# Kernel optimization log

Hardware: AMD Instinct MI355X
Metric: run time of the kernel (lower is better)

Reference implementation:

```python
import jax, jax.numpy as jnp
import numpy as np

B, P, H, D = 32, 384, 384, 512
DA, DC, DH, NUM_LABELS = 512, 512, 512, 3


def setup_inputs() -> dict:
    key = jax.random.key(0)
    ks = jax.random.split(key, 12)
    s = lambda d: 1.0 / np.sqrt(d)
    return {
        "embedded_premise": jax.random.normal(ks[0], (B, P, D), jnp.float32),
        "embedded_hypothesis": jax.random.normal(ks[1], (B, H, D), jnp.float32),
        "premise_mask": jax.random.randint(ks[2], (B, P), 0, 2, jnp.int32),
        "hypothesis_mask": jax.random.randint(ks[3], (B, H), 0, 2, jnp.int32),
        "W_attend": jax.random.normal(ks[4], (D, DA), jnp.float32) * s(D),
        "b_attend": jnp.zeros((DA,), jnp.float32),
        "W_compare": jax.random.normal(ks[5], (2 * D, DC), jnp.float32) * s(2 * D),
        "b_compare": jnp.zeros((DC,), jnp.float32),
        "W_agg1": jax.random.normal(ks[6], (2 * DC, DH), jnp.float32) * s(2 * DC),
        "b_agg1": jnp.zeros((DH,), jnp.float32),
        "W_agg2": jax.random.normal(ks[7], (DH, NUM_LABELS), jnp.float32) * s(DH),
        "b_agg2": jnp.zeros((NUM_LABELS,), jnp.float32),
    }


def masked_softmax(scores, mask):
    # AllenNLP (legacy, non-memory-efficient) masked_softmax:
    # softmax(scores * mask), re-mask, renormalize with epsilon.
    result = jax.nn.softmax(scores * mask, axis=-1)
    result = result * mask
    return result / (jnp.sum(result, axis=-1, keepdims=True) + 1e-13)


def reference(embedded_premise, embedded_hypothesis, premise_mask, hypothesis_mask,
              W_attend, b_attend, W_compare, b_compare,
              W_agg1, b_agg1, W_agg2, b_agg2):
    pm = premise_mask.astype(jnp.float32)      # [B, P]
    hm = hypothesis_mask.astype(jnp.float32)   # [B, H]

    # TimeDistributed attend feedforward (shared weights)
    proj_p = jax.nn.relu(embedded_premise @ W_attend + b_attend)      # [B, P, DA]
    proj_h = jax.nn.relu(embedded_hypothesis @ W_attend + b_attend)   # [B, H, DA]

    # Dot-product similarity matrix [B, P, H]
    sim = jnp.einsum('bpd,bhd->bph', proj_p, proj_h)

    # Cross attention with masked softmax
    p2h = masked_softmax(sim, hm[:, None, :])                          # [B, P, H]
    attended_hypothesis = jnp.einsum('bph,bhd->bpd', p2h, embedded_hypothesis)
    h2p = masked_softmax(jnp.swapaxes(sim, 1, 2), pm[:, None, :])      # [B, H, P]
    attended_premise = jnp.einsum('bhp,bpd->bhd', h2p, embedded_premise)

    # Compare feedforward on concatenated inputs, then masked sum over time
    cmp_p = jax.nn.relu(
        jnp.concatenate([embedded_premise, attended_hypothesis], axis=-1) @ W_compare + b_compare)
    compared_premise = jnp.sum(cmp_p * pm[:, :, None], axis=1)         # [B, DC]
    cmp_h = jax.nn.relu(
        jnp.concatenate([embedded_hypothesis, attended_premise], axis=-1) @ W_compare + b_compare)
    compared_hypothesis = jnp.sum(cmp_h * hm[:, :, None], axis=1)      # [B, DC]

    # Aggregate feedforward
    agg = jnp.concatenate([compared_premise, compared_hypothesis], axis=-1)
    hidden = jax.nn.relu(agg @ W_agg1 + b_agg1)
    label_logits = hidden @ W_agg2 + b_agg2                            # [B, NUM_LABELS]
    label_probs = jax.nn.softmax(label_logits, axis=-1)
    return label_logits, label_probs, h2p, p2h
```

## Files before the change

kernel.cpp:

```cpp
#include <hip/hip_runtime.h>
#include <hip/hip_bf16.h>
#include <math.h>

typedef __bf16 bf16_t;
typedef __bf16 bf16x8 __attribute__((ext_vector_type(8)));
typedef float f32x4 __attribute__((ext_vector_type(4)));

#define NPH 12288
#define SIM_B (384*384)
#define EMB_B (384*512)

#define OUT_LOGITS 0
#define OUT_PROBS 96
#define OUT_H2P 192
#define OUT_P2H (192 + 32*384*384)

#define OFF_WATH 0L
#define OFF_WATL 524288L
#define OFF_WCT  1048576L
#define OFF_A    2097152L
#define OFF_SIM  52428800L
#define OFF_CM   71303168L
#define OFF_CS   (OFF_CM + 49152L)
#define OFF_GP   (OFF_CS + 49152L)
#define OFF_H    (OFF_GP + 524288L)

#define PROJ_LO   6291456L
#define PROJ_Z    12582912L
#define ATT_ALL_E 12582912L
#define CMP_Z     6291456L

#define BM 128
#define BN 128
#define BKK 32

#define M_PROJ   0
#define M_SPLITB 1
#define M_PLAIN  2
#define M_CONCAT 3
#define O_F32   0
#define O_BF16  1
#define O_SPLIT 2
#define O_GSUM  3

__device__ inline void gload16(const void* g, void* l) {
    __builtin_amdgcn_global_load_lds(
        (const __attribute__((address_space(1))) void*)g,
        (__attribute__((address_space(3))) void*)l, 16, 0, 0);
}

template<bool SPLIT>
__device__ inline void stage_sw(const float* __restrict__ s,
                                bf16_t* hi, bf16_t* lo, int row, int c0)
{
    float xs[16];
    *(float4*)&xs[0]  = *(const float4*)(s);
    *(float4*)&xs[4]  = *(const float4*)(s + 4);
    *(float4*)&xs[8]  = *(const float4*)(s + 8);
    *(float4*)&xs[12] = *(const float4*)(s + 12);
    bf16x8 h0, h1, l0, l1;
    #pragma unroll
    for (int i = 0; i < 8; i++) {
        float x = xs[i];     bf16_t hh = (bf16_t)x; h0[i] = hh;
        float y = xs[i + 8]; bf16_t hy = (bf16_t)y; h1[i] = hy;
        if (SPLIT) { l0[i] = (bf16_t)(x - (float)hh); l1[i] = (bf16_t)(y - (float)hy); }
    }
    const int key = (row >> 1) & 3;
    const int cc0 = c0 ^ key, cc1 = cc0 ^ 1;
    *(bf16x8*)&hi[row * 32 + cc0 * 8] = h0;
    *(bf16x8*)&hi[row * 32 + cc1 * 8] = h1;
    if (SPLIT) {
        *(bf16x8*)&lo[row * 32 + cc0 * 8] = l0;
        *(bf16x8*)&lo[row * 32 + cc1 * 8] = l1;
    }
}

template<int MODE, int OUTK, bool BIAS, bool RELU>
__global__ __launch_bounds__(256) void mgemm(
    const float* __restrict__ Af, const float* __restrict__ Af2, int zalt,
    const bf16_t* __restrict__ Abh, long loA,
    const bf16_t* __restrict__ A2b, long a2B,
    const bf16_t* __restrict__ Bbh, long loB,
    const float* __restrict__ bias,
    const int* __restrict__ pmask, const int* __restrict__ hmask,
    float* __restrict__ Cf, bf16_t* __restrict__ Cb, long loC,
    int K, int K1,
    long aB, long bB, long cB,
    int lda, int lda2, int ldb, int ldc)
{
    constexpr int NS = (MODE == M_PROJ || MODE == M_SPLITB) ? 2 : 1;
    __shared__ bf16_t As[NS][BM * BKK];
    __shared__ bf16_t Bs[NS][BM * BKK];

    const int tid = threadIdx.x;

    const int gx = gridDim.x, gy = gridDim.y;
    const int nwg = gx * gy * gridDim.z;
    int flat = blockIdx.x + gx * (blockIdx.y + gy * blockIdx.z);
    flat = (flat & 7) * (nwg >> 3) + (flat >> 3);
    const int bz_ = flat / (gx * gy);
    const int rem_ = flat - bz_ * (gx * gy);
    const int by_ = rem_ / gx, bx_ = rem_ - by_ * gx;

    const long z = bz_;
    const int m0 = by_ * BM, n0 = bx_ * BN;

    const float* Afs = (MODE == M_PROJ || MODE == M_PLAIN || MODE == M_CONCAT)
                       ? ((z >= zalt) ? Af2 : Af) : nullptr;

    const int sr = tid >> 1, sc = (tid & 1) * 16, c0 = (tid & 1) * 2;
    const int gr = tid >> 2;
    const int gco = ((tid & 3) ^ ((gr >> 1) & 3)) * 8;
    const int wlds = (tid >> 6) * 512;

    const int l = tid & 63;
    const int wv = tid >> 6;
    const int wr = (wv >> 1) * 64, wc = (wv & 1) * 64;
    const int fr = l & 15, fq = l >> 4;

    f32x4 acc[4][4] = {};

    for (int k0 = 0; k0 < K; k0 += BKK) {
        if (MODE == M_PROJ || MODE == M_PLAIN) {
            const float* s = Afs + z * aB + (long)(m0 + sr) * lda + k0 + sc;
            stage_sw<MODE == M_PROJ>(s, As[0], As[NS - 1], sr, c0);
        } else if (MODE == M_CONCAT) {
            if (k0 < K1) {
                const float* s = Afs + z * aB + (long)(m0 + sr) * lda + k0 + sc;
                stage_sw<false>(s, As[0], nullptr, sr, c0);
            } else {
                const bf16_t* s = A2b + z * a2B + (long)(m0 + gr) * lda2 + (k0 - K1) + gco;
                gload16(s, &As[0][wlds]);
                gload16(s + (long)64 * lda2, &As[0][2048 + wlds]);
            }
        } else {
            const bf16_t* s = Abh + z * aB + (long)(m0 + gr) * lda + k0 + gco;
            gload16(s, &As[0][wlds]);
            gload16(s + (long)64 * lda, &As[0][2048 + wlds]);
            gload16(s + loA, &As[NS - 1][wlds]);
            gload16(s + loA + (long)64 * lda, &As[NS - 1][2048 + wlds]);
        }
        {
            const bf16_t* s = Bbh + z * bB + (long)(n0 + gr) * ldb + k0 + gco;
            gload16(s, &Bs[0][wlds]);
            gload16(s + (long)64 * ldb, &Bs[0][2048 + wlds]);
            if (NS == 2) {
                gload16(s + loB, &Bs[NS - 1][wlds]);
                gload16(s + loB + (long)64 * ldb, &Bs[NS - 1][2048 + wlds]);
            }
        }
        __syncthreads();

        bf16x8 a_h[4], b_h[4], a_l[4], b_l[4];
        #pragma unroll
        for (int i = 0; i < 4; i++) {
            const int ra = wr + i * 16 + fr;
            const int rb = wc + i * 16 + fr;
            const int ka = (fq ^ ((ra >> 1) & 3)) * 8;
            const int kb = (fq ^ ((rb >> 1) & 3)) * 8;
            a_h[i] = *(const bf16x8*)&As[0][ra * 32 + ka];
            b_h[i] = *(const bf16x8*)&Bs[0][rb * 32 + kb];
            if (NS == 2) {
                a_l[i] = *(const bf16x8*)&As[NS - 1][ra * 32 + ka];
                b_l[i] = *(const bf16x8*)&Bs[NS - 1][rb * 32 + kb];
            }
        }
        #pragma unroll
        for (int mi = 0; mi < 4; mi++)
            #pragma unroll
            for (int ni = 0; ni < 4; ni++) {
                acc[mi][ni] = __builtin_amdgcn_mfma_f32_16x16x32_bf16(a_h[mi], b_h[ni], acc[mi][ni], 0, 0, 0);
                if (NS == 2) {
                    acc[mi][ni] = __builtin_amdgcn_mfma_f32_16x16x32_bf16(a_h[mi], b_l[ni], acc[mi][ni], 0, 0, 0);
                    acc[mi][ni] = __builtin_amdgcn_mfma_f32_16x16x32_bf16(a_l[mi], b_h[ni], acc[mi][ni], 0, 0, 0);
                }
            }
        __syncthreads();
    }

    if constexpr (OUTK == O_GSUM) {
        __shared__ float red[8][128];
        __shared__ int smask[128];
        const int* mrow = (z >= zalt) ? hmask : pmask;
        const int bb = m0 / 384;
        const int brow0 = m0 - bb * 384;
        if (tid < 128) smask[tid] = mrow[bb * 384 + brow0 + tid];
        __syncthreads();
        const int rid = (wv >> 1) * 4 + fq;
        #pragma unroll
        for (int ni = 0; ni < 4; ni++) {
            const int c = wc + ni * 16 + fr;
            const float bv = bias[n0 + c];
            float local = 0.f;
            #pragma unroll
            for (int mi = 0; mi < 4; mi++)
                #pragma unroll
                for (int j = 0; j < 4; j++) {
                    const int rloc = wr + mi * 16 + fq * 4 + j;
                    float v = fmaxf(acc[mi][ni][j] + bv, 0.f);
                    local += v * (float)smask[rloc];
                }
            red[rid][c] = local;
        }
        __syncthreads();
        if (tid < 128) {
            float s = 0.f;
            #pragma unroll
            for (int r = 0; r < 8; r++) s += red[r][tid];
            const int pc = (m0 >> 7) % 3;
            Cf[((long)pc * 32 + bb) * 1024 + z * 512 + n0 + tid] = s;
        }
    } else {
        #pragma unroll
        for (int ni = 0; ni < 4; ni++) {
            const int col = n0 + wc + ni * 16 + fr;
            const float bv = BIAS ? bias[col] : 0.f;
            #pragma unroll
            for (int mi = 0; mi < 4; mi++) {
                #pragma unroll
                for (int j = 0; j < 4; j++) {
                    const int row = m0 + wr + mi * 16 + fq * 4 + j;
                    float v = acc[mi][ni][j] + bv;
                    if (RELU) v = fmaxf(v, 0.f);
                    const long idx = z * cB + (long)row * ldc + col;
                    if (OUTK == O_F32) Cf[idx] = v;
                    else if (OUTK == O_BF16) Cb[idx] = (bf16_t)v;
                    else {
                        bf16_t h = (bf16_t)v;
                        Cb[idx] = h;
                        Cb[idx + loC] = (bf16_t)(v - (float)h);
                    }
                }
            }
        }
    }
}

template<bool SPLIT>
__global__ __launch_bounds__(256) void transpose_kernel(
    const float* __restrict__ in, const float* __restrict__ in2, int zsplit,
    bf16_t* __restrict__ out, bf16_t* __restrict__ outLo,
    int R, int C, long inB, long outB)
{
    __shared__ float tile[32][33];
    const int z = blockIdx.z;
    const float* src = (z >= zsplit) ? (in2 + (long)(z - zsplit) * inB)
                                     : (in + (long)z * inB);
    const int x0 = blockIdx.x * 32, y0 = blockIdx.y * 32;
    const int tx = threadIdx.x & 31, ty = threadIdx.x >> 5;
    #pragma unroll
    for (int i = 0; i < 32; i += 8)
        tile[ty + i][tx] = src[(long)(y0 + ty + i) * C + x0 + tx];
    __syncthreads();
    bf16_t* dst = out + (long)z * outB;
    bf16_t* dstL = SPLIT ? (outLo + (long)z * outB) : nullptr;
    #pragma unroll
    for (int i = 0; i < 32; i += 8) {
        float v = tile[tx][ty + i];
        bf16_t h = (bf16_t)v;
        dst[(long)(x0 + ty + i) * R + y0 + tx] = h;
        if (SPLIT) dstL[(long)(x0 + ty + i) * R + y0 + tx] = (bf16_t)(v - (float)h);
    }
}

__global__ __launch_bounds__(384) void masked_softmax_row(
    const float* __restrict__ S, const int* __restrict__ mask,
    float* __restrict__ out)
{
    const int row = blockIdx.x;
    const int b = row / 384;
    const int t = threadIdx.x;
    __shared__ float redmax[6], redsum[6];

    float v = S[(long)row * 384 + t];
    int mm = mask[b * 384 + t];

    float x = mm ? v : -3.4e38f;
    #pragma unroll
    for (int o = 32; o > 0; o >>= 1) x = fmaxf(x, __shfl_xor(x, o, 64));
    int wid = t >> 6, lane = t & 63;
    if (lane == 0) redmax[wid] = x;
    __syncthreads();
    float mx = redmax[0];
    #pragma unroll
    for (int w = 1; w < 6; w++) mx = fmaxf(mx, redmax[w]);

    float e = mm ? expf(v - mx) : 0.f;
    float s = e;
    #pragma unroll
    for (int o = 32; o > 0; o >>= 1) s += __shfl_xor(s, o, 64);
    if (lane == 0) redsum[wid] = s;
    __syncthreads();
    float tot = 0.f;
    #pragma unroll
    for (int w = 0; w < 6; w++) tot += redsum[w];

    out[(long)row * 384 + t] = (tot > 0.f) ? e / tot : 0.f;
}

__global__ __launch_bounds__(256) void col_stats(
    const float* __restrict__ S, const int* __restrict__ mask,
    float* __restrict__ cmax, float* __restrict__ csum)
{
    __shared__ int pml[384];
    __shared__ float mred[4][64], sred[4][64];
    const int b = blockIdx.y;
    const int h0 = blockIdx.x * 64;
    const int t = threadIdx.x;
    const int tk = t >> 6, hh = t & 63;

    for (int i = t; i < 384; i += 256) pml[i] = mask[b * 384 + i];
    __syncthreads();

    const float* Sb = S + (long)b * SIM_B + h0 + hh;
    float m = -3.4e38f;
    for (int p = tk; p < 384; p += 4)
        if (pml[p]) m = fmaxf(m, Sb[(long)p * 384]);
    mred[tk][hh] = m;
    __syncthreads();
    const float M = fmaxf(fmaxf(mred[0][hh], mred[1][hh]),
                          fmaxf(mred[2][hh], mred[3][hh]));
    float s = 0.f;
    for (int p = tk; p < 384; p += 4)
        if (pml[p]) s += expf(Sb[(long)p * 384] - M);
    sred[tk][hh] = s;
    __syncthreads();
    if (t < 64) {
        const float Mf = fmaxf(fmaxf(mred[0][t], mred[1][t]),
                               fmaxf(mred[2][t], mred[3][t]));
        cmax[b * 384 + h0 + t] = Mf;
        csum[b * 384 + h0 + t] = sred[0][t] + sred[1][t] + sred[2][t] + sred[3][t];
    }
}

__global__ __launch_bounds__(256) void col_write(
    const float* __restrict__ S, const int* __restrict__ mask,
    const float* __restrict__ cmax, const float* __restrict__ csum,
    float* __restrict__ out)
{
    __shared__ float tile[32][33];
    const int b = blockIdx.z;
    const int h0 = blockIdx.x * 32, p0 = blockIdx.y * 32;
    const int tx = threadIdx.x & 31, ty = threadIdx.x >> 5;
    const float* src = S + (long)b * SIM_B;
    #pragma unroll
    for (int i = 0; i < 32; i += 8)
        tile[ty + i][tx] = src[(long)(p0 + ty + i) * 384 + h0 + tx];
    __syncthreads();
    const int pm_v = mask[b * 384 + p0 + tx];
    float* dst = out + (long)b * SIM_B;
    #pragma unroll
    for (int i = 0; i < 32; i += 8) {
        const int h = h0 + ty + i;
        const float mx = cmax[b * 384 + h];
        const float tot = csum[b * 384 + h];
        float v = tile[tx][ty + i];
        float r = (pm_v && tot > 0.f) ? expf(v - mx) / tot : 0.f;
        dst[(long)h * 384 + p0 + tx] = r;
    }
}

__global__ __launch_bounds__(256) void hidden_kernel(
    const float* __restrict__ Gp, const float* __restrict__ W1,
    const float* __restrict__ b1, float* __restrict__ Hbuf)
{
    __shared__ float g[1024];
    __shared__ float part[4][64];
    const int b = blockIdx.y, j0 = blockIdx.x * 64;
    const int t = threadIdx.x;
    for (int i = t; i < 1024; i += 256)
        g[i] = Gp[((long)0 * 32 + b) * 1024 + i] + Gp[((long)1 * 32 + b) * 1024 + i]
             + Gp[((long)2 * 32 + b) * 1024 + i];
    __syncthreads();
    const int tj = t & 63, tk = t >> 6;
    const float* w = W1 + (long)(tk * 256) * 512 + j0 + tj;
    const float* gk = g + tk * 256;
    float acc = 0.f;
    #pragma unroll 8
    for (int k = 0; k < 256; k++)
        acc = fmaf(gk[k], w[(long)k * 512], acc);
    part[tk][tj] = acc;
    __syncthreads();
    if (t < 64) {
        float v = part[0][t] + part[1][t] + part[2][t] + part[3][t] + b1[j0 + t];
        Hbuf[(long)b * 512 + j0 + t] = fmaxf(v, 0.f);
    }
}

__global__ __launch_bounds__(64) void logits_kernel(
    const float* __restrict__ Hbuf, const float* __restrict__ W2,
    const float* __restrict__ b2, float* __restrict__ out)
{
    const int b = blockIdx.x, l = threadIdx.x;
    const float* h = Hbuf + (long)b * 512;
    float a0 = 0.f, a1 = 0.f, a2 = 0.f;
    #pragma unroll
    for (int k = l; k < 512; k += 64) {
        float hv = h[k];
        a0 = fmaf(hv, W2[k * 3 + 0], a0);
        a1 = fmaf(hv, W2[k * 3 + 1], a1);
        a2 = fmaf(hv, W2[k * 3 + 2], a2);
    }
    #pragma unroll
    for (int o = 32; o > 0; o >>= 1) {
        a0 += __shfl_xor(a0, o, 64);
        a1 += __shfl_xor(a1, o, 64);
        a2 += __shfl_xor(a2, o, 64);
    }
    if (l == 0) {
        float l0 = a0 + b2[0], l1 = a1 + b2[1], l2 = a2 + b2[2];
        float mx = fmaxf(l0, fmaxf(l1, l2));
        float e0 = expf(l0 - mx), e1 = expf(l1 - mx), e2 = expf(l2 - mx);
        float s = e0 + e1 + e2;
        out[OUT_LOGITS + b * 3 + 0] = l0;
        out[OUT_LOGITS + b * 3 + 1] = l1;
        out[OUT_LOGITS + b * 3 + 2] = l2;
        out[OUT_PROBS + b * 3 + 0] = e0 / s;
        out[OUT_PROBS + b * 3 + 1] = e1 / s;
        out[OUT_PROBS + b * 3 + 2] = e2 / s;
    }
}

extern "C" void kernel_launch(void* const* d_in, const int* in_sizes, int n_in,
                              void* d_out, int out_size, void* d_ws, size_t ws_size,
                              hipStream_t stream) {
    const float* emb_p = (const float*)d_in[0];
    const float* emb_h = (const float*)d_in[1];
    const int* pm = (const int*)d_in[2];
    const int* hm = (const int*)d_in[3];
    const float* Wa = (const float*)d_in[4];
    const float* ba = (const float*)d_in[5];
    const float* Wc = (const float*)d_in[6];
    const float* bc = (const float*)d_in[7];
    const float* W1 = (const float*)d_in[8];
    const float* b1 = (const float*)d_in[9];
    const float* W2 = (const float*)d_in[10];
    const float* b2 = (const float*)d_in[11];
    float* out = (float*)d_out;
    char* W = (char*)d_ws;

    bf16_t* WaTh  = (bf16_t*)(W + OFF_WATH);
    bf16_t* WaTl  = (bf16_t*)(W + OFF_WATL);
    bf16_t* WcT   = (bf16_t*)(W + OFF_WCT);
    bf16_t* A     = (bf16_t*)(W + OFF_A);
    float*  sim   = (float*)(W + OFF_SIM);
    float*  cmaxb = (float*)(W + OFF_CM);
    float*  csumb = (float*)(W + OFF_CS);
    float*  Gp    = (float*)(W + OFF_GP);
    float*  Hbuf  = (float*)(W + OFF_H);
    bf16_t* projs  = A;
    bf16_t* embT   = A;
    bf16_t* attAll = A + ATT_ALL_E;

    transpose_kernel<true><<<dim3(16, 16, 1), 256, 0, stream>>>(
        Wa, nullptr, 999, WaTh, WaTl, 512, 512, 0, 0);
    transpose_kernel<false><<<dim3(16, 32, 1), 256, 0, stream>>>(
        Wc, nullptr, 999, WcT, nullptr, 1024, 512, 0, 0);

    mgemm<M_PROJ, O_SPLIT, true, true><<<dim3(4, 96, 2), 256, 0, stream>>>(
        emb_p, emb_h, 1, nullptr, 0, nullptr, 0, WaTh, 262144L, ba,
        nullptr, nullptr,
        nullptr, projs, PROJ_LO,
        512, 0, 0L, 0L, PROJ_Z, 512, 0, 512, 512);

    mgemm<M_SPLITB, O_F32, false, false><<<dim3(3, 3, 32), 256, 0, stream>>>(
        nullptr, nullptr, 999, projs, PROJ_LO, nullptr, 0,
        projs + PROJ_Z, PROJ_LO, nullptr,
        nullptr, nullptr,
        sim, nullptr, 0,
        512, 0, (long)EMB_B, (long)EMB_B, (long)SIM_B, 512, 0, 512, 384);

    masked_softmax_row<<<NPH, 384, 0, stream>>>(sim, hm, out + OUT_P2H);
    col_stats<<<dim3(6, 32), 256, 0, stream>>>(sim, pm, cmaxb, csumb);
    col_write<<<dim3(12, 12, 32), 256, 0, stream>>>(sim, pm, cmaxb, csumb, out + OUT_H2P);

    transpose_kernel<false><<<dim3(16, 12, 64), 256, 0, stream>>>(
        emb_p, emb_h, 32, embT, nullptr, 384, 512, (long)EMB_B, (long)EMB_B);

    mgemm<M_PLAIN, O_BF16, false, false><<<dim3(4, 3, 64), 256, 0, stream>>>(
        out + OUT_H2P, nullptr, 1 << 30, nullptr, 0, nullptr, 0,
        embT, 0, nullptr,
        nullptr, nullptr,
        nullptr, attAll, 0,
        384, 0, (long)SIM_B, (long)EMB_B, (long)EMB_B, 384, 0, 384, 512);

    mgemm<M_CONCAT, O_GSUM, true, true><<<dim3(4, 96, 2), 256, 0, stream>>>(
        emb_p, emb_h, 1, nullptr, 0,
        attAll + CMP_Z, -(long)CMP_Z,
        WcT, 0, bc,
        pm, hm,
        Gp, nullptr, 0,
        1024, 512, 0L, 0L, 0L, 512, 512, 1024, 512);

    hidden_kernel<<<dim3(8, 32), 256, 0, stream>>>(Gp, W1, b1, Hbuf);
    logits_kernel<<<32, 64, 0, stream>>>(Hbuf, W2, b2, out);
}
```

Baseline: 380.9 us.

## Split-K the similarity GEMM with atomics and stage bf16 epilogue stores through LDS

```diff
diff --git a/kernel.cpp b/kernel.cpp
--- a/kernel.cpp
+++ b/kernel.cpp
@@ -75,7 +75,7 @@
     }
 }
 
-template<int MODE, int OUTK, bool BIAS, bool RELU>
+template<int MODE, int OUTK, bool BIAS, bool RELU, bool KSPLIT = false>
 __global__ __launch_bounds__(256) void mgemm(
     const float* __restrict__ Af, const float* __restrict__ Af2, int zalt,
     const bf16_t* __restrict__ Abh, long loA,
@@ -89,8 +89,12 @@
     int lda, int lda2, int ldb, int ldc)
 {
     constexpr int NS = (MODE == M_PROJ || MODE == M_SPLITB) ? 2 : 1;
-    __shared__ bf16_t As[NS][BM * BKK];
-    __shared__ bf16_t Bs[NS][BM * BKK];
+    constexpr bool REPACK = (OUTK == O_SPLIT || OUTK == O_BF16);
+    constexpr int SM_ELEMS = REPACK ? ((NS * 8192 > 17408) ? NS * 8192 : 17408)
+                                    : NS * 8192;
+    __shared__ bf16_t smem[SM_ELEMS];
+    bf16_t* As = smem;
+    bf16_t* Bs = smem + NS * 4096;
 
     const int tid = threadIdx.x;
 
@@ -103,10 +107,12 @@
     const int by_ = rem_ / gx, bx_ = rem_ - by_ * gx;
 
     const long z = bz_;
+    const long zb = KSPLIT ? (z >> 1) : z;
+    const int koff = KSPLIT ? (int)(z & 1) * K : 0;
     const int m0 = by_ * BM, n0 = bx_ * BN;
 
     const float* Afs = (MODE == M_PROJ || MODE == M_PLAIN || MODE == M_CONCAT)
-                       ? ((z >= zalt) ? Af2 : Af) : nullptr;
+                       ? ((zb >= zalt) ? Af2 : Af) : nullptr;
 
     const int sr = tid >> 1, sc = (tid & 1) * 16, c0 = (tid & 1) * 2;
     const int gr = tid >> 2;
@@ -121,32 +127,33 @@
     f32x4 acc[4][4] = {};
 
     for (int k0 = 0; k0 < K; k0 += BKK) {
+        const int kk = koff + k0;
         if (MODE == M_PROJ || MODE == M_PLAIN) {
-            const float* s = Afs + z * aB + (long)(m0 + sr) * lda + k0 + sc;
-            stage_sw<MODE == M_PROJ>(s, As[0], As[NS - 1], sr, c0);
+            const float* s = Afs + zb * aB + (long)(m0 + sr) * lda + kk + sc;
+            stage_sw<MODE == M_PROJ>(s, As, As + (NS - 1) * 4096, sr, c0);
         } else if (MODE == M_CONCAT) {
             if (k0 < K1) {
-                const float* s = Afs + z * aB + (long)(m0 + sr) * lda + k0 + sc;
-                stage_sw<false>(s, As[0], nullptr, sr, c0);
+                const float* s = Afs + zb * aB + (long)(m0 + sr) * lda + kk + sc;
+                stage_sw<false>(s, As, nullptr, sr, c0);
             } else {
-                const bf16_t* s = A2b + z * a2B + (long)(m0 + gr) * lda2 + (k0 - K1) + gco;
-                gload16(s, &As[0][wlds]);
-                gload16(s + (long)64 * lda2, &As[0][2048 + wlds]);
+                const bf16_t* s = A2b + zb * a2B + (long)(m0 + gr) * lda2 + (kk - K1) + gco;
+                gload16(s, As + wlds);
+                gload16(s + (long)64 * lda2, As + 2048 + wlds);
             }
         } else {
-            const bf16_t* s = Abh + z * aB + (long)(m0 + gr) * lda + k0 + gco;
-            gload16(s, &As[0][wlds]);
-            gload16(s + (long)64 * lda, &As[0][2048 + wlds]);
-            gload16(s + loA, &As[NS - 1][wlds]);
-            gload16(s + loA + (long)64 * lda, &As[NS - 1][2048 + wlds]);
+            const bf16_t* s = Abh + zb * aB + (long)(m0 + gr) * lda + kk + gco;
+            gload16(s, As + wlds);
+            gload16(s + (long)64 * lda, As + 2048 + wlds);
+            gload16(s + loA, As + (NS - 1) * 4096 + wlds);
+            gload16(s + loA + (long)64 * lda, As + (NS - 1) * 4096 + 2048 + wlds);
         }
         {
-            const bf16_t* s = Bbh + z * bB + (long)(n0 + gr) * ldb + k0 + gco;
-            gload16(s, &Bs[0][wlds]);
-            gload16(s + (long)64 * ldb, &Bs[0][2048 + wlds]);
+            const bf16_t* s = Bbh + zb * bB + (long)(n0 + gr) * ldb + kk + gco;
+            gload16(s, Bs + wlds);
+            gload16(s + (long)64 * ldb, Bs + 2048 + wlds);
             if (NS == 2) {
-                gload16(s + loB, &Bs[NS - 1][wlds]);
-                gload16(s + loB + (long)64 * ldb, &Bs[NS - 1][2048 + wlds]);
+                gload16(s + loB, Bs + (NS - 1) * 4096 + wlds);
+                gload16(s + loB + (long)64 * ldb, Bs + (NS - 1) * 4096 + 2048 + wlds);
             }
         }
         __syncthreads();
@@ -158,11 +165,11 @@
             const int rb = wc + i * 16 + fr;
             const int ka = (fq ^ ((ra >> 1) & 3)) * 8;
             const int kb = (fq ^ ((rb >> 1) & 3)) * 8;
-            a_h[i] = *(const bf16x8*)&As[0][ra * 32 + ka];
-            b_h[i] = *(const bf16x8*)&Bs[0][rb * 32 + kb];
+            a_h[i] = *(const bf16x8*)&As[ra * 32 + ka];
+            b_h[i] = *(const bf16x8*)&Bs[rb * 32 + kb];
             if (NS == 2) {
-                a_l[i] = *(const bf16x8*)&As[NS - 1][ra * 32 + ka];
-                b_l[i] = *(const bf16x8*)&Bs[NS - 1][rb * 32 + kb];
+                a_l[i] = *(const bf16x8*)&As[(NS - 1) * 4096 + ra * 32 + ka];
+                b_l[i] = *(const bf16x8*)&Bs[(NS - 1) * 4096 + rb * 32 + kb];
             }
         }
         #pragma unroll
@@ -181,7 +188,7 @@
     if constexpr (OUTK == O_GSUM) {
         __shared__ float red[8][128];
         __shared__ int smask[128];
-        const int* mrow = (z >= zalt) ? hmask : pmask;
+        const int* mrow = (zb >= zalt) ? hmask : pmask;
         const int bb = m0 / 384;
         const int brow0 = m0 - bb * 384;
         if (tid < 128) smask[tid] = mrow[bb * 384 + brow0 + tid];
@@ -208,7 +215,36 @@
             #pragma unroll
             for (int r = 0; r < 8; r++) s += red[r][tid];
             const int pc = (m0 >> 7) % 3;
-            Cf[((long)pc * 32 + bb) * 1024 + z * 512 + n0 + tid] = s;
+            Cf[((long)pc * 32 + bb) * 1024 + zb * 512 + n0 + tid] = s;
+        }
+    } else if constexpr (REPACK) {
+        const int prow = tid >> 1;
+        const int pcol0 = (tid & 1) * 64;
+        #pragma unroll
+        for (int r = 0; r < (OUTK == O_SPLIT ? 2 : 1); r++) {
+            __syncthreads();
+            #pragma unroll
+            for (int ni = 0; ni < 4; ni++) {
+                const int c = wc + ni * 16 + fr;
+                const float bv = BIAS ? bias[n0 + c] : 0.f;
+                #pragma unroll
+                for (int mi = 0; mi < 4; mi++)
+                    #pragma unroll
+                    for (int j = 0; j < 4; j++) {
+                        const int row = wr + mi * 16 + fq * 4 + j;
+                        float v = acc[mi][ni][j] + bv;
+                        if (RELU) v = fmaxf(v, 0.f);
+                        bf16_t h = (bf16_t)v;
+                        smem[row * 136 + c] = (r == 0) ? h : (bf16_t)(v - (float)h);
+                    }
+            }
+            __syncthreads();
+            #pragma unroll
+            for (int i = 0; i < 8; i++) {
+                bf16x8 w = *(const bf16x8*)&smem[prow * 136 + pcol0 + i * 8];
+                *(bf16x8*)&Cb[zb * cB + (long)(m0 + prow) * ldc + n0 + pcol0 + i * 8
+                              + (r ? loC : 0L)] = w;
+            }
         }
     } else {
         #pragma unroll
@@ -222,14 +258,9 @@
                     const int row = m0 + wr + mi * 16 + fq * 4 + j;
                     float v = acc[mi][ni][j] + bv;
                     if (RELU) v = fmaxf(v, 0.f);
-                    const long idx = z * cB + (long)row * ldc + col;
-                    if (OUTK == O_F32) Cf[idx] = v;
-                    else if (OUTK == O_BF16) Cb[idx] = (bf16_t)v;
-                    else {
-                        bf16_t h = (bf16_t)v;
-                        Cb[idx] = h;
-                        Cb[idx + loC] = (bf16_t)(v - (float)h);
-                    }
+                    const long idx = zb * cB + (long)row * ldc + col;
+                    if (KSPLIT) atomicAdd(&Cf[idx], v);
+                    else        Cf[idx] = v;
                 }
             }
         }
@@ -463,12 +494,13 @@
         nullptr, projs, PROJ_LO,
         512, 0, 0L, 0L, PROJ_Z, 512, 0, 512, 512);
 
-    mgemm<M_SPLITB, O_F32, false, false><<<dim3(3, 3, 32), 256, 0, stream>>>(
+    hipMemsetAsync(sim, 0, 18874368L, stream);
+    mgemm<M_SPLITB, O_F32, false, false, true><<<dim3(3, 3, 64), 256, 0, stream>>>(
         nullptr, nullptr, 999, projs, PROJ_LO, nullptr, 0,
         projs + PROJ_Z, PROJ_LO, nullptr,
         nullptr, nullptr,
         sim, nullptr, 0,
-        512, 0, (long)EMB_B, (long)EMB_B, (long)SIM_B, 512, 0, 512, 384);
+        256, 0, (long)EMB_B, (long)EMB_B, (long)SIM_B, 512, 0, 512, 384);
 
     masked_softmax_row<<<NPH, 384, 0, stream>>>(sim, hm, out + OUT_P2H);
     col_stats<<<dim3(6, 32), 256, 0, stream>>>(sim, pm, cmaxb, csumb);
```

Measured after the change: 429.3 us. 12.7% more time.
